# Performance work log

Measured on AMD Instinct MI355X. Metric: run time of the kernel, lower is better.

The kernel has to match this reference:

```python
import jax, jax.numpy as jnp
import numpy as np
from functools import partial

# ---- module hyperparameters (from init_kwargs) ----
INP_DIM = 128
OUT_DIM = 128
NOISE_LEVEL = 0.1
AB_MVM = 8   # activation bits after MVM
IB = 8       # input activation bits
WB = 8       # weight bits
BATCH = 262144


def step_d(bits):
    return 2.0 ** (bits - 1)


def pact_a(x, a):
    # PACT clip: sign(x) * 0.5 * (|x| - ||x| - a| + a)
    return jnp.sign(x) * 0.5 * (jnp.abs(x) - jnp.abs(jnp.abs(x) - a) + a)


@partial(jax.custom_vjp, nondiff_argnums=(2,))
def quant_ste(x, x_range, bits):
    # fake-quantize x to `bits` bits over [-x_range, x_range], straight-through grad
    sd = step_d(bits)
    x01 = jnp.clip(x / x_range, -1.0 + 1.0 / sd, 1.0 - 1.0 / sd)
    return jnp.round(x01 * sd) / sd * x_range


def _quant_fwd(x, x_range, bits):
    return quant_ste(x, x_range, bits), x_range


def _quant_bwd(bits, x_range, g):
    # torch QuantFunc.backward: grad passes straight through to x, None for range
    return (g, jnp.zeros_like(x_range))


quant_ste.defvjp(_quant_fwd, _quant_bwd)


def _noisy_mm(x, w, b):
    # simulated analog MVM: quantized weights + per-tensor Gaussian noise
    k1, k2 = jax.random.split(jax.random.key(1234))
    noise_w = jax.random.normal(k1, w.shape, w.dtype) * w.max() * NOISE_LEVEL
    noise_b = jax.random.normal(k2, b.shape, b.dtype) * b.max() * NOISE_LEVEL
    wq = quant_ste(w, 1.0, WB)
    bq = quant_ste(b, 1.0, WB)
    return x @ (wq + noise_w) + bq + noise_b


custom_mm = jax.custom_vjp(_noisy_mm)


def _mm_fwd(x, w, b):
    return _noisy_mm(x, w, b), (x, w)


def _mm_bwd(res, g):
    # torch CustomMM.backward uses CLEAN (un-noised, un-quantized) weight/input
    x, w = res
    return (g @ w.T, x.T @ g, g.sum(0))


custom_mm.defvjp(_mm_fwd, _mm_bwd)


def setup_inputs() -> dict:
    key = jax.random.key(0)
    kx, kw = jax.random.split(key)
    x = jax.random.normal(kx, (BATCH, INP_DIM), dtype=jnp.float32)
    # weight init: uniform(-limit, limit) with limit = max(sqrt(6/inp_dim), 1.5/2^(wb-1))
    limit = max(np.sqrt(6.0 / INP_DIM), 1.5 / (2.0 ** (WB - 1)))
    weights = jax.random.uniform(kw, (INP_DIM, OUT_DIM), dtype=jnp.float32,
                                 minval=-limit, maxval=limit)
    bias = jnp.zeros((OUT_DIM,), dtype=jnp.float32)  # torch init: uniform(0, 0)
    a1 = jnp.array([4.0], dtype=jnp.float32)
    a2 = jnp.array([16.0], dtype=jnp.float32)
    return {"x": x, "weights": weights, "bias": bias, "a1": a1, "a2": a2}


def reference(x, weights, bias, a1, a2):
    # quant_pass(pact_a(CustomMM(quant_pass(pact_a(x,a1), ib, a1), W, b, nl, wb), a2), abMVM, a2)
    xq = quant_ste(pact_a(x, a1), a1, IB)          # [B, inp_dim]
    h = custom_mm(xq, weights, bias)               # [B, out_dim]
    return quant_ste(pact_a(h, a2), a2, AB_MVM)    # [B, out_dim]
```

## Files before the change

kernel.cpp:

```cpp
#include <hip/hip_runtime.h>
#include <stdint.h>

#define INP 128
#define OUTD 128
#define WT_STRIDE 136
#define XT_STRIDE 132
#define THREEFRY_PARTITIONABLE 1

typedef __bf16 bf16x8 __attribute__((ext_vector_type(8)));
typedef float  floatx4 __attribute__((ext_vector_type(4)));

__device__ __forceinline__ uint32_t rotl32(uint32_t v, uint32_t n) {
  return (v << n) | (v >> (32u - n));
}
__device__ __forceinline__ void tf_round(uint32_t& x0, uint32_t& x1, uint32_t r) {
  x0 += x1; x1 = rotl32(x1, r); x1 ^= x0;
}
__device__ void threefry2x32(uint32_t k0, uint32_t k1, uint32_t c0, uint32_t c1,
                             uint32_t& o0, uint32_t& o1) {
  uint32_t k2 = k0 ^ k1 ^ 0x1BD11BDAu;
  uint32_t x0 = c0 + k0, x1 = c1 + k1;
  tf_round(x0,x1,13); tf_round(x0,x1,15); tf_round(x0,x1,26); tf_round(x0,x1,6);
  x0 += k1; x1 += k2 + 1u;
  tf_round(x0,x1,17); tf_round(x0,x1,29); tf_round(x0,x1,16); tf_round(x0,x1,24);
  x0 += k2; x1 += k0 + 2u;
  tf_round(x0,x1,13); tf_round(x0,x1,15); tf_round(x0,x1,26); tf_round(x0,x1,6);
  x0 += k0; x1 += k1 + 3u;
  tf_round(x0,x1,17); tf_round(x0,x1,29); tf_round(x0,x1,16); tf_round(x0,x1,24);
  x0 += k1; x1 += k2 + 4u;
  tf_round(x0,x1,13); tf_round(x0,x1,15); tf_round(x0,x1,26); tf_round(x0,x1,6);
  x0 += k2; x1 += k0 + 5u;
  o0 = x0; o1 = x1;
}

__device__ float erfinv_giles(float x) {
  float w = -logf((1.0f - x) * (1.0f + x));
  float p;
  if (w < 5.0f) {
    w = w - 2.5f;
    p = 2.81022636e-08f;
    p = fmaf(p, w, 3.43273939e-07f);
    p = fmaf(p, w, -3.5233877e-06f);
    p = fmaf(p, w, -4.39150654e-06f);
    p = fmaf(p, w, 0.00021858087f);
    p = fmaf(p, w, -0.00125372503f);
    p = fmaf(p, w, -0.00417768164f);
    p = fmaf(p, w, 0.246640727f);
    p = fmaf(p, w, 1.50140941f);
  } else {
    w = sqrtf(w) - 3.0f;
    p = -0.000200214257f;
    p = fmaf(p, w, 0.000100950558f);
    p = fmaf(p, w, 0.00134934322f);
    p = fmaf(p, w, -0.00367342844f);
    p = fmaf(p, w, 0.00573950773f);
    p = fmaf(p, w, -0.0076224613f);
    p = fmaf(p, w, 0.00943887047f);
    p = fmaf(p, w, 1.00167406f);
    p = fmaf(p, w, 2.83297682f);
  }
  return p * x;
}

__device__ float normal_from_bits(uint32_t bits) {
  const float lo = -0.999999940395355224609375f;
  uint32_t fb = (bits >> 9) | 0x3F800000u;
  float f = __uint_as_float(fb) - 1.0f;
  float u = fmaxf(lo, f * 2.0f + lo);
  return 1.41421356237309515f * erfinv_giles(u);
}

__device__ __forceinline__ uint32_t rand_bits(uint32_t ka, uint32_t kb, int i, int half) {
#if THREEFRY_PARTITIONABLE
  (void)half;
  uint32_t o0, o1;
  threefry2x32(ka, kb, 0u, (uint32_t)i, o0, o1);
  return o0 ^ o1;
#else
  uint32_t c0 = (i < half) ? (uint32_t)i : (uint32_t)(i - half);
  uint32_t o0, o1;
  threefry2x32(ka, kb, c0, c0 + (uint32_t)half, o0, o1);
  return (i < half) ? o0 : o1;
#endif
}

__global__ __launch_bounds__(256) void setup_reduce(
    const float* __restrict__ w, const float* __restrict__ bias,
    float* __restrict__ biasEff, float* __restrict__ scalars) {
  __shared__ float red[8];
  const int tid = threadIdx.x;

  float m = -3.4e38f;
  for (int i = tid; i < INP * OUTD; i += 256) m = fmaxf(m, w[i]);
  #pragma unroll
  for (int off = 1; off < 64; off <<= 1) m = fmaxf(m, __shfl_xor(m, off));
  float bm = (tid < OUTD) ? bias[tid] : -3.4e38f;
  #pragma unroll
  for (int off = 1; off < 64; off <<= 1) bm = fmaxf(bm, __shfl_xor(bm, off));
  if ((tid & 63) == 0) { red[tid >> 6] = m; red[4 + (tid >> 6)] = bm; }
  __syncthreads();
  const float wmax = fmaxf(fmaxf(red[0], red[1]), fmaxf(red[2], red[3]));
  const float bmax = fmaxf(fmaxf(red[4], red[5]), fmaxf(red[6], red[7]));
  if (tid == 0) { scalars[0] = wmax; scalars[1] = bmax; }

  uint32_t k2a, k2b;
#if THREEFRY_PARTITIONABLE
  threefry2x32(0u, 1234u, 0u, 1u, k2a, k2b);
#else
  { uint32_t a0, b0, a1, b1;
    threefry2x32(0u, 1234u, 0u, 2u, a0, b0);
    threefry2x32(0u, 1234u, 1u, 3u, a1, b1);
    k2a = b0; k2b = b1; }
#endif
  if (tid < OUTD) {
    float nrm = normal_from_bits(rand_bits(k2a, k2b, tid, OUTD / 2));
    float bv = bias[tid];
    float bq = rintf(fminf(fmaxf(bv * 128.f, -127.f), 127.f)) * 0.0078125f;
    biasEff[tid] = bq + (nrm * bmax) * 0.1f;
  }
}

__global__ __launch_bounds__(256) void setup_noise(
    const float* __restrict__ w, __bf16* __restrict__ wt,
    const float* __restrict__ scalars) {
  const int i = blockIdx.x * 256 + threadIdx.x;
  const float wmax = scalars[0];

  uint32_t k1a, k1b;
#if THREEFRY_PARTITIONABLE
  threefry2x32(0u, 1234u, 0u, 0u, k1a, k1b);
#else
  { uint32_t a0, b0, a1, b1;
    threefry2x32(0u, 1234u, 0u, 2u, a0, b0);
    threefry2x32(0u, 1234u, 1u, 3u, a1, b1);
    k1a = a0; k1b = a1; }
#endif

  float nrm = normal_from_bits(rand_bits(k1a, k1b, i, (INP * OUTD) / 2));
  int r = i >> 7, c = i & 127;
  float wv = w[i];
  float wq = rintf(fminf(fmaxf(wv * 128.f, -127.f), 127.f)) * 0.0078125f;
  wt[c * WT_STRIDE + r] = (__bf16)(wq + (nrm * wmax) * 0.1f);
}

__device__ __forceinline__ void load_tile_contig(floatx4 v[8], const float* __restrict__ x,
                                                 long tile, int lane) {
  const float* p = x + ((size_t)tile << 11) + lane * 4;
  #pragma unroll
  for (int k = 0; k < 8; ++k) v[k] = *(const floatx4*)(p + k * 256);
}

__device__ __forceinline__ void stage_tile(const floatx4 v[8], float* __restrict__ myX,
                                           int lane) {
  const int r0 = lane >> 5;
  const int c  = (lane & 31) * 4;
  #pragma unroll
  for (int k = 0; k < 8; ++k)
    *(floatx4*)&myX[(2 * k + r0) * XT_STRIDE + c] = v[k];
}

__device__ __forceinline__ bf16x8 quant_pair(floatx4 v0, floatx4 v1, float s1, float r1) {
  bf16x8 a;
  #pragma unroll
  for (int i = 0; i < 4; ++i) {
    a[i]     = (__bf16)(rintf(fminf(fmaxf(v0[i] * s1, -127.f), 127.f)) * r1);
    a[i + 4] = (__bf16)(rintf(fminf(fmaxf(v1[i] * s1, -127.f), 127.f)) * r1);
  }
  return a;
}

__device__ __forceinline__ void compute_tile(
    const float* __restrict__ myX, const __bf16* sW, const float* sBias,
    float* __restrict__ out, long tile, int n16, int quad,
    float s1, float r1, float s2, float r2) {
  floatx4 acc[8];
  #pragma unroll
  for (int ct = 0; ct < 8; ++ct) acc[ct] = (floatx4)0.0f;

  #pragma unroll
  for (int kc = 0; kc < 4; ++kc) {
    const float* fr = &myX[n16 * XT_STRIDE + kc * 32 + quad * 8];
    floatx4 f0 = *(const floatx4*)fr;
    floatx4 f1 = *(const floatx4*)(fr + 4);
    bf16x8 a = quant_pair(f0, f1, s1, r1);
    const int kOff = kc * 32 + quad * 8;
    #pragma unroll
    for (int ct = 0; ct < 8; ++ct) {
      bf16x8 wfrag = *(const bf16x8*)&sW[(ct * 16 + n16) * WT_STRIDE + kOff];
      acc[ct] = __builtin_amdgcn_mfma_f32_16x16x32_bf16(wfrag, a, acc[ct], 0, 0, 0);
    }
  }

  float* orow = out + ((size_t)(tile * 16 + n16) << 7);
  #pragma unroll
  for (int ct = 0; ct < 8; ++ct) {
    const int colBase = ct * 16 + quad * 4;
    floatx4 o;
    #pragma unroll
    for (int r = 0; r < 4; ++r) {
      float h = acc[ct][r] + sBias[colBase + r];
      float t = fminf(fmaxf(h * s2, -127.0f), 127.0f);
      o[r] = rintf(t) * r2;
    }
    *(floatx4*)(orow + colBase) = o;
  }
}

__global__ __launch_bounds__(256) void linlayer_main(
    const float* __restrict__ x, const __bf16* __restrict__ wt,
    const float* __restrict__ biasEff, const float* __restrict__ a1p,
    const float* __restrict__ a2p, float* __restrict__ out, int nTiles) {
  __shared__ __attribute__((aligned(16))) __bf16 sW[OUTD * WT_STRIDE];
  __shared__ __attribute__((aligned(16))) float sX[4][16 * XT_STRIDE];
  __shared__ float sBias[OUTD];

  const int tid  = threadIdx.x;
  const int wave = tid >> 6;
  const int lane = tid & 63;
  const int n16  = lane & 15;
  const int quad = lane >> 4;

  const int nWaves = gridDim.x * 4;
  const int waveId = blockIdx.x * 4 + wave;
  const long last  = nTiles - 1;

  floatx4 bufA[8], bufB[8];
  long t = waveId;
  load_tile_contig(bufA, x, (t <= last) ? t : last, lane);

  {
    const uint4* src = (const uint4*)wt;
    uint4* dst = (uint4*)sW;
    for (int i = tid; i < (OUTD * WT_STRIDE * 2) / 16; i += 256) dst[i] = src[i];
  }
  if (tid < OUTD) sBias[tid] = biasEff[tid];

  const float a1 = a1p[0], a2 = a2p[0];
  const float s1 = 128.0f / a1, r1 = a1 * 0.0078125f;
  const float s2 = 128.0f / a2, r2 = a2 * 0.0078125f;

  __syncthreads();

  float* myX = sX[wave];

  while (t <= last) {
    long tn = t + nWaves;
    load_tile_contig(bufB, x, (tn <= last) ? tn : last, lane);
    stage_tile(bufA, myX, lane);
    compute_tile(myX, sW, sBias, out, t, n16, quad, s1, r1, s2, r2);
    t = tn;
    if (t > last) break;

    tn = t + nWaves;
    load_tile_contig(bufA, x, (tn <= last) ? tn : last, lane);
    stage_tile(bufB, myX, lane);
    compute_tile(myX, sW, sBias, out, t, n16, quad, s1, r1, s2, r2);
    t = tn;
  }
}

extern "C" void kernel_launch(void* const* d_in, const int* in_sizes, int n_in,
                              void* d_out, int out_size, void* d_ws, size_t ws_size,
                              hipStream_t stream) {
  const float* x    = (const float*)d_in[0];
  const float* w    = (const float*)d_in[1];
  const float* bias = (const float*)d_in[2];
  const float* a1   = (const float*)d_in[3];
  const float* a2   = (const float*)d_in[4];
  float* out = (float*)d_out;

  __bf16* wt     = (__bf16*)d_ws;
  float* biasEff = (float*)((char*)d_ws + OUTD * WT_STRIDE * 2);
  float* scalars = (float*)((char*)d_ws + OUTD * WT_STRIDE * 2 + 512);

  const int rows   = in_sizes[0] / INP;
  const int nTiles = rows / 16;
  const int grid   = 512;

  setup_reduce<<<1, 256, 0, stream>>>(w, bias, biasEff, scalars);
  setup_noise<<<64, 256, 0, stream>>>(w, wt, scalars);
  linlayer_main<<<grid, 256, 0, stream>>>(x, wt, biasEff, a1, a2, out, nTiles);
}
```

Before: 267.8 us.

## Fuse setup kernels, store quantized bf16 input tile in LDS, raise occupancy

Merges the two setup kernels into one, with every block recomputing the weight max redundantly, which removes a launch and a dependency. Input activations are now quantized and converted to bf16 once while staging into shared memory, instead of being stored as fp32 and requantized in each MFMA k-chunk. That halves the LDS footprint and traffic for the X tile. Launch bounds now request 3 blocks per CU and the grid grows from 512 to 768 persistent blocks to raise occupancy, at the risk of register pressure.

```diff
diff --git a/kernel.cpp b/kernel.cpp
--- a/kernel.cpp
+++ b/kernel.cpp
@@ -4,10 +4,10 @@
 #define INP 128
 #define OUTD 128
 #define WT_STRIDE 136
-#define XT_STRIDE 132
-#define THREEFRY_PARTITIONABLE 1
+#define XT_STRIDE 136
 
 typedef __bf16 bf16x8 __attribute__((ext_vector_type(8)));
+typedef __bf16 bf16x4 __attribute__((ext_vector_type(4)));
 typedef float  floatx4 __attribute__((ext_vector_type(4)));
 
 __device__ __forceinline__ uint32_t rotl32(uint32_t v, uint32_t n) {
@@ -70,77 +70,58 @@
   return 1.41421356237309515f * erfinv_giles(u);
 }
 
-__device__ __forceinline__ uint32_t rand_bits(uint32_t ka, uint32_t kb, int i, int half) {
-#if THREEFRY_PARTITIONABLE
-  (void)half;
+__device__ __forceinline__ uint32_t rand_bits(uint32_t ka, uint32_t kb, int i) {
   uint32_t o0, o1;
   threefry2x32(ka, kb, 0u, (uint32_t)i, o0, o1);
   return o0 ^ o1;
-#else
-  uint32_t c0 = (i < half) ? (uint32_t)i : (uint32_t)(i - half);
-  uint32_t o0, o1;
-  threefry2x32(ka, kb, c0, c0 + (uint32_t)half, o0, o1);
-  return (i < half) ? o0 : o1;
-#endif
-}
-
-__global__ __launch_bounds__(256) void setup_reduce(
+}
+
+__global__ __launch_bounds__(256) void setup_fused(
     const float* __restrict__ w, const float* __restrict__ bias,
-    float* __restrict__ biasEff, float* __restrict__ scalars) {
+    __bf16* __restrict__ wt, float* __restrict__ biasEff) {
   __shared__ float red[8];
   const int tid = threadIdx.x;
 
-  float m = -3.4e38f;
-  for (int i = tid; i < INP * OUTD; i += 256) m = fmaxf(m, w[i]);
+  const floatx4* w4 = (const floatx4*)w;
+  float m0 = -3.4e38f, m1 = m0, m2 = m0, m3 = m0;
+  #pragma unroll
+  for (int it = 0; it < 16; ++it) {
+    floatx4 v = w4[it * 256 + tid];
+    m0 = fmaxf(m0, v[0]); m1 = fmaxf(m1, v[1]);
+    m2 = fmaxf(m2, v[2]); m3 = fmaxf(m3, v[3]);
+  }
+  float m = fmaxf(fmaxf(m0, m1), fmaxf(m2, m3));
   #pragma unroll
   for (int off = 1; off < 64; off <<= 1) m = fmaxf(m, __shfl_xor(m, off));
-  float bm = (tid < OUTD) ? bias[tid] : -3.4e38f;
-  #pragma unroll
-  for (int off = 1; off < 64; off <<= 1) bm = fmaxf(bm, __shfl_xor(bm, off));
-  if ((tid & 63) == 0) { red[tid >> 6] = m; red[4 + (tid >> 6)] = bm; }
+  if ((tid & 63) == 0) red[tid >> 6] = m;
   __syncthreads();
   const float wmax = fmaxf(fmaxf(red[0], red[1]), fmaxf(red[2], red[3]));
-  const float bmax = fmaxf(fmaxf(red[4], red[5]), fmaxf(red[6], red[7]));
-  if (tid == 0) { scalars[0] = wmax; scalars[1] = bmax; }
-
-  uint32_t k2a, k2b;
-#if THREEFRY_PARTITIONABLE
-  threefry2x32(0u, 1234u, 0u, 1u, k2a, k2b);
-#else
-  { uint32_t a0, b0, a1, b1;
-    threefry2x32(0u, 1234u, 0u, 2u, a0, b0);
-    threefry2x32(0u, 1234u, 1u, 3u, a1, b1);
-    k2a = b0; k2b = b1; }
-#endif
-  if (tid < OUTD) {
-    float nrm = normal_from_bits(rand_bits(k2a, k2b, tid, OUTD / 2));
-    float bv = bias[tid];
-    float bq = rintf(fminf(fmaxf(bv * 128.f, -127.f), 127.f)) * 0.0078125f;
-    biasEff[tid] = bq + (nrm * bmax) * 0.1f;
-  }
-}
-
-__global__ __launch_bounds__(256) void setup_noise(
-    const float* __restrict__ w, __bf16* __restrict__ wt,
-    const float* __restrict__ scalars) {
-  const int i = blockIdx.x * 256 + threadIdx.x;
-  const float wmax = scalars[0];
 
   uint32_t k1a, k1b;
-#if THREEFRY_PARTITIONABLE
   threefry2x32(0u, 1234u, 0u, 0u, k1a, k1b);
-#else
-  { uint32_t a0, b0, a1, b1;
-    threefry2x32(0u, 1234u, 0u, 2u, a0, b0);
-    threefry2x32(0u, 1234u, 1u, 3u, a1, b1);
-    k1a = a0; k1b = a1; }
-#endif
-
-  float nrm = normal_from_bits(rand_bits(k1a, k1b, i, (INP * OUTD) / 2));
+  const int i = blockIdx.x * 256 + tid;
+  float nrm = normal_from_bits(rand_bits(k1a, k1b, i));
   int r = i >> 7, c = i & 127;
   float wv = w[i];
   float wq = rintf(fminf(fmaxf(wv * 128.f, -127.f), 127.f)) * 0.0078125f;
   wt[c * WT_STRIDE + r] = (__bf16)(wq + (nrm * wmax) * 0.1f);
+
+  if (blockIdx.x == 0) {
+    float bv = (tid < OUTD) ? bias[tid] : -3.4e38f;
+    float bm = bv;
+    #pragma unroll
+    for (int off = 1; off < 64; off <<= 1) bm = fmaxf(bm, __shfl_xor(bm, off));
+    if ((tid & 63) == 0) red[4 + (tid >> 6)] = bm;
+    __syncthreads();
+    const float bmax = fmaxf(fmaxf(red[4], red[5]), fmaxf(red[6], red[7]));
+    if (tid < OUTD) {
+      uint32_t k2a, k2b;
+      threefry2x32(0u, 1234u, 0u, 1u, k2a, k2b);
+      float nrm2 = normal_from_bits(rand_bits(k2a, k2b, tid));
+      float bq = rintf(fminf(fmaxf(bv * 128.f, -127.f), 127.f)) * 0.0078125f;
+      biasEff[tid] = bq + (nrm2 * bmax) * 0.1f;
+    }
+  }
 }
 
 __device__ __forceinline__ void load_tile_contig(floatx4 v[8], const float* __restrict__ x,
@@ -150,40 +131,32 @@
   for (int k = 0; k < 8; ++k) v[k] = *(const floatx4*)(p + k * 256);
 }
 
-__device__ __forceinline__ void stage_tile(const floatx4 v[8], float* __restrict__ myX,
-                                           int lane) {
+__device__ __forceinline__ void stage_tile_q(const floatx4 v[8], __bf16* __restrict__ myX,
+                                             int lane, float s1, float r1) {
   const int r0 = lane >> 5;
   const int c  = (lane & 31) * 4;
   #pragma unroll
-  for (int k = 0; k < 8; ++k)
-    *(floatx4*)&myX[(2 * k + r0) * XT_STRIDE + c] = v[k];
-}
-
-__device__ __forceinline__ bf16x8 quant_pair(floatx4 v0, floatx4 v1, float s1, float r1) {
-  bf16x8 a;
-  #pragma unroll
-  for (int i = 0; i < 4; ++i) {
-    a[i]     = (__bf16)(rintf(fminf(fmaxf(v0[i] * s1, -127.f), 127.f)) * r1);
-    a[i + 4] = (__bf16)(rintf(fminf(fmaxf(v1[i] * s1, -127.f), 127.f)) * r1);
-  }
-  return a;
+  for (int k = 0; k < 8; ++k) {
+    bf16x4 q;
+    #pragma unroll
+    for (int j = 0; j < 4; ++j)
+      q[j] = (__bf16)(rintf(fminf(fmaxf(v[k][j] * s1, -127.f), 127.f)) * r1);
+    *(bf16x4*)&myX[(2 * k + r0) * XT_STRIDE + c] = q;
+  }
 }
 
 __device__ __forceinline__ void compute_tile(
-    const float* __restrict__ myX, const __bf16* sW, const float* sBias,
+    const __bf16* __restrict__ myX, const __bf16* sW, const float* sBias,
     float* __restrict__ out, long tile, int n16, int quad,
-    float s1, float r1, float s2, float r2) {
+    float s2, float r2) {
   floatx4 acc[8];
   #pragma unroll
   for (int ct = 0; ct < 8; ++ct) acc[ct] = (floatx4)0.0f;
 
   #pragma unroll
   for (int kc = 0; kc < 4; ++kc) {
-    const float* fr = &myX[n16 * XT_STRIDE + kc * 32 + quad * 8];
-    floatx4 f0 = *(const floatx4*)fr;
-    floatx4 f1 = *(const floatx4*)(fr + 4);
-    bf16x8 a = quant_pair(f0, f1, s1, r1);
     const int kOff = kc * 32 + quad * 8;
+    bf16x8 a = *(const bf16x8*)&myX[n16 * XT_STRIDE + kOff];
     #pragma unroll
     for (int ct = 0; ct < 8; ++ct) {
       bf16x8 wfrag = *(const bf16x8*)&sW[(ct * 16 + n16) * WT_STRIDE + kOff];
@@ -199,19 +172,19 @@
     #pragma unroll
     for (int r = 0; r < 4; ++r) {
       float h = acc[ct][r] + sBias[colBase + r];
-      float t = fminf(fmaxf(h * s2, -127.0f), 127.0f);
-      o[r] = rintf(t) * r2;
+      float tq = fminf(fmaxf(h * s2, -127.0f), 127.0f);
+      o[r] = rintf(tq) * r2;
     }
     *(floatx4*)(orow + colBase) = o;
   }
 }
 
-__global__ __launch_bounds__(256) void linlayer_main(
+__global__ __launch_bounds__(256, 3) void linlayer_main(
     const float* __restrict__ x, const __bf16* __restrict__ wt,
     const float* __restrict__ biasEff, const float* __restrict__ a1p,
     const float* __restrict__ a2p, float* __restrict__ out, int nTiles) {
   __shared__ __attribute__((aligned(16))) __bf16 sW[OUTD * WT_STRIDE];
-  __shared__ __attribute__((aligned(16))) float sX[4][16 * XT_STRIDE];
+  __shared__ __attribute__((aligned(16))) __bf16 sX[4][16 * XT_STRIDE];
   __shared__ float sBias[OUTD];
 
   const int tid  = threadIdx.x;
@@ -241,20 +214,20 @@
 
   __syncthreads();
 
-  float* myX = sX[wave];
+  __bf16* myX = sX[wave];
 
   while (t <= last) {
     long tn = t + nWaves;
     load_tile_contig(bufB, x, (tn <= last) ? tn : last, lane);
-    stage_tile(bufA, myX, lane);
-    compute_tile(myX, sW, sBias, out, t, n16, quad, s1, r1, s2, r2);
+    stage_tile_q(bufA, myX, lane, s1, r1);
+    compute_tile(myX, sW, sBias, out, t, n16, quad, s2, r2);
     t = tn;
     if (t > last) break;
 
     tn = t + nWaves;
     load_tile_contig(bufA, x, (tn <= last) ? tn : last, lane);
-    stage_tile(bufB, myX, lane);
-    compute_tile(myX, sW, sBias, out, t, n16, quad, s1, r1, s2, r2);
+    stage_tile_q(bufB, myX, lane, s1, r1);
+    compute_tile(myX, sW, sBias, out, t, n16, quad, s2, r2);
     t = tn;
   }
 }
@@ -271,13 +244,11 @@
 
   __bf16* wt     = (__bf16*)d_ws;
   float* biasEff = (float*)((char*)d_ws + OUTD * WT_STRIDE * 2);
-  float* scalars = (float*)((char*)d_ws + OUTD * WT_STRIDE * 2 + 512);
 
   const int rows   = in_sizes[0] / INP;
   const int nTiles = rows / 16;
-  const int grid   = 512;
-
-  setup_reduce<<<1, 256, 0, stream>>>(w, bias, biasEff, scalars);
-  setup_noise<<<64, 256, 0, stream>>>(w, wt, scalars);
+  const int grid   = 768;
+
+  setup_fused<<<64, 256, 0, stream>>>(w, bias, wt, biasEff);
   linlayer_main<<<grid, 256, 0, stream>>>(x, wt, biasEff, a1, a2, out, nTiles);
 }
```

New measurement: 301.0 us. 12.4% more time.
